# Kernel optimization log

Hardware: AMD Instinct MI355X
Metric: run time of the kernel (lower is better)

The kernel has to match this reference:

```python
import jax, jax.numpy as jnp
import numpy as np

THRESH = 1.0
TAU_M = 20.0
TAU_S = 5.0
NUM_STEPS = 300
LENS = 0.5  # boxcar surrogate half-width for the spike Heaviside

@jax.custom_vjp
def act_fun(x):
    # Heaviside spike with boxcar surrogate gradient (as in BPTC-NOSO ActFun)
    return (x > 0.0).astype(x.dtype)

def _act_fwd(x):
    return act_fun(x), x

def _act_bwd(x, g):
    return (g * (jnp.abs(x) < LENS).astype(g.dtype),)

act_fun.defvjp(_act_fwd, _act_bwd)

@jax.custom_vjp
def dodt(spike, dt):
    # forward: spike * (step - num_steps); backward: surrogate do/dt = -spike
    return spike * dt

def _dodt_fwd(spike, dt):
    return spike * dt, spike

def _dodt_bwd(spike, g):
    return (-g * spike, jnp.zeros((), g.dtype))

dodt.defvjp(_dodt_fwd, _dodt_bwd)

def setup_inputs() -> dict:
    key = jax.random.key(0)
    k1, k2, k3 = jax.random.split(key, 3)
    B = 256
    N_IN, N_H, N_OUT = 2 * 34 * 34, 800, 10
    # binary event spikes like N-MNIST (sparse-ish)
    inp = (jax.random.uniform(k1, (B, 2, 34, 34, NUM_STEPS)) < 0.1).astype(jnp.float32)
    w1 = jax.random.normal(k2, (N_H, N_IN), jnp.float32) * np.float32(np.sqrt(2.0 / N_IN))
    w2 = jax.random.normal(k3, (N_OUT, N_H), jnp.float32) * np.float32(np.sqrt(2.0 / N_H))
    return {"input": inp, "w1": w1, "w2": w2, "batch_size": B}

def _forward(input, w1, w2, batch_size):
    B = batch_size
    N_IN, N_H, N_OUT = w1.shape[1], w1.shape[0], w2.shape[0]
    dm = jnp.float32(np.exp(-1.0 / TAU_M))
    ds = jnp.float32(np.exp(-1.0 / TAU_S))
    x_t = jnp.moveaxis(input.reshape(B, N_IN, NUM_STEPS), -1, 0)  # [T, B, N_IN]

    z = lambda n: jnp.zeros((B, n), jnp.float32)
    o = lambda n: jnp.ones((B, n), jnp.float32)
    carry = (z(N_IN), z(N_IN), o(N_H),          # vm1, vs1, sav1
             z(N_H), z(N_H), o(N_OUT),          # vm2, vs2, sav2
             NUM_STEPS * jnp.ones((B, N_OUT), jnp.float32),  # out_t
             z(N_OUT),                           # out_u
             jnp.zeros((3,), jnp.float32))       # sum_sp

    def step(c, xs):
        vm1, vs1, sav1, vm2, vs2, sav2, out_t, out_u, sum_sp = c
        step_f, in_spike = xs
        # layer 1: dual-exponential synapse traces on input, NOSO (one spike) gating
        vm1 = dm * vm1 + in_spike
        vs1 = ds * vs1 + in_spike
        u1 = sav1 * ((vm1 - vs1) @ w1.T)        # um - us fused into one GEMM
        spk1 = act_fun(u1 - THRESH)
        sav1 = sav1 * (1.0 - spk1)
        # layer 2 (output neurons)
        vm2 = dm * vm2 + spk1
        vs2 = ds * vs2 + spk1
        u2 = sav2 * ((vm2 - vs2) @ w2.T)
        spk2 = act_fun(u2 - THRESH)
        sav2 = sav2 * (1.0 - spk2)
        out_t = out_t + dodt(spk2, step_f - NUM_STEPS)  # records first-spike time
        out_u = out_u + spk2 * u2
        sum_sp = sum_sp + jax.lax.stop_gradient(
            jnp.stack([in_spike.sum(), spk1.sum(), spk2.sum()]))
        return (vm1, vs1, sav1, vm2, vs2, sav2, out_t, out_u, sum_sp), None

    steps = jnp.arange(NUM_STEPS, dtype=jnp.float32)
    c, _ = jax.lax.scan(step, carry, (steps, x_t))
    return c[6], c[7], c[8]

def reference(input, w1, w2, batch_size):
    return _forward(input, w1, w2, batch_size)
```

## Files before the change

### kernel.cpp

```cpp
#include <hip/hip_runtime.h>
#include <hip/hip_bf16.h>

typedef unsigned int u32;
typedef unsigned short u16;

#define BATCH 256
#define TSTEPS 300
#define N_IN 2312
#define N_H 800
#define N_OUT 10
#define KW 74
#define KREAL 2368
#define KSTEPS 74
#define MTOT (BATCH * TSTEPS)
#define ROWB 9472

#define BM 128
#define BN 160

typedef __attribute__((ext_vector_type(8))) short bf16x8;
typedef __attribute__((ext_vector_type(4))) float f32x4;

static inline size_t alignup(size_t x) { return (x + 255) & ~(size_t)255; }

__device__ __forceinline__ void gl_lds16(const void* g, void* l) {
    __builtin_amdgcn_global_load_lds(
        (const __attribute__((address_space(1))) unsigned int*)g,
        (__attribute__((address_space(3))) unsigned int*)l,
        16, 0, 0);
}

__global__ void init_k(u32* cnts) {
    if (threadIdx.x < 4) cnts[threadIdx.x] = 0;
}

__global__ __launch_bounds__(256) void prep_w(const float* __restrict__ w1,
                                              u32* __restrict__ Wc) {
    int idx = blockIdx.x * 256 + threadIdx.x;
    if (idx >= N_H * KREAL) return;
    int h = idx / KREAL, k = idx - h * KREAL;
    float w = (k < N_IN) ? w1[(size_t)h * N_IN + k] : 0.0f;
    __hip_bfloat16 hb = __float2bfloat16(w);
    float hf = __bfloat162float(hb);
    __hip_bfloat16 lb = __float2bfloat16(w - hf);
    u32 val = (u32)(*(u16*)&hb) | ((u32)(*(u16*)&lb) << 16);
    Wc[(size_t)h * KREAL + k] = val;
}

__global__ __launch_bounds__(256) void prep_x(const float* __restrict__ X,
                                              u32* __restrict__ XB,
                                              u32* __restrict__ cnts,
                                              int b0) {
    int bl = blockIdx.x;
    int b = b0 + bl;
    int tc = blockIdx.y;
    int t0 = tc * 64;
    int nrows = min(64, TSTEPS - t0);
    __shared__ u32 bits[64][76];
    int tid = threadIdx.x;
    int tl = tid & 63;
    int wg = tid >> 6;
    int t = t0 + tl;
    bool tvalid = (tl < nrows);
    u32 pc = 0;
    for (int j = 0; j < 19; ++j) {
        int w = wg + 4 * j;
        if (w >= KW) break;
        u32 reg = 0;
        if (w < 73 && tvalid) {
            int ibase = w * 32;
            int nb = min(32, N_IN - ibase);
            const float* xp = X + ((size_t)b * N_IN + ibase) * TSTEPS + t;
            for (int bit = 0; bit < nb; ++bit) {
                float v = xp[(size_t)bit * TSTEPS];
                reg |= (v > 0.5f) ? (1u << bit) : 0u;
            }
        }
        pc += __popc(reg);
        bits[tl][w] = reg;
    }
    for (int off = 32; off; off >>= 1) pc += __shfl_down(pc, off);
    if ((tid & 63) == 0 && pc) atomicAdd(cnts + 0, pc);
    __syncthreads();
    int total = nrows * KW;
    u32* outp = XB + (size_t)(bl * TSTEPS + t0) * KW;
    for (int idx = tid; idx < total; idx += 256) {
        int r = idx / KW, w = idx - r * KW;
        outp[idx] = bits[r][w];
    }
}

__global__ __launch_bounds__(256, 4) void gemm_k(const u32* __restrict__ XB,
                                                 const u16* __restrict__ Wc,
                                                 float* __restrict__ C1,
                                                 int nwg, int mblocks) {
    int d = blockIdx.y * 5 + blockIdx.x;
    int xcd = d & 7, jj = d >> 3;
    int q = nwg >> 3, r = nwg & 7;
    int lid = (xcd < r ? xcd * (q + 1) : r * (q + 1) + (xcd - r) * q) + jj;
    int nb = lid / mblocks, mb = lid - nb * mblocks;
    int m0 = mb * BM, n0 = nb * BN;

    __shared__ __align__(16) u16 Bs[2][BN * 64];

    int tid = threadIdx.x, lane = tid & 63, w = tid >> 6;
    int wm = w >> 1, wn = w & 1;

    const char* srcB[5];
#pragma unroll
    for (int i = 0; i < 5; ++i) {
        int slot = w * 5120 + i * 1024 + lane * 16;
        int row = slot >> 7, c = (slot >> 4) & 7;
        srcB[i] = (const char*)Wc + (size_t)(n0 + row) * ROWB + (size_t)((c ^ (row & 7)) << 4);
    }
    char* ldsB = (char*)&Bs[0][0] + w * 5120;

    int r0 = wm * 64 + (lane & 15);
    const u32* pAm0 = XB + (size_t)(m0 + r0) * KW;
    const u32* pAm1 = pAm0 + 16 * KW;
    const u32* pAm2 = pAm0 + 32 * KW;
    const u32* pAm3 = pAm0 + 48 * KW;
    int sh0 = (lane >> 4) * 4;

    f32x4 acc[4][5] = {};

#pragma unroll
    for (int i = 0; i < 5; ++i) { gl_lds16(srcB[i], ldsB + i * 1024); srcB[i] += 128; }
    __syncthreads();

    for (int ks = 0; ks < KSTEPS; ++ks) {
        int buf = ks & 1;
        if (ks < KSTEPS - 1) {
            char* dst = ldsB + (buf ^ 1) * 20480;
#pragma unroll
            for (int i = 0; i < 5; ++i) { gl_lds16(srcB[i], dst + i * 1024); srcB[i] += 128; }
        }
        u32 wv0 = pAm0[ks], wv1 = pAm1[ks], wv2 = pAm2[ks], wv3 = pAm3[ks];
        const u16* bsb = &Bs[buf][0];
#pragma unroll
        for (int kk = 0; kk < 2; ++kk) {
            u32 wv[4] = {wv0, wv1, wv2, wv3};
            bf16x8 af[4];
#pragma unroll
            for (int mi = 0; mi < 4; ++mi) {
                u32 nib = wv[mi] >> (kk * 16 + sh0);
                uint4 ax;
                ax.x = (nib & 1u) ? 0x3F803F80u : 0u;
                ax.y = (nib & 2u) ? 0x3F803F80u : 0u;
                ax.z = (nib & 4u) ? 0x3F803F80u : 0u;
                ax.w = (nib & 8u) ? 0x3F803F80u : 0u;
                af[mi] = *reinterpret_cast<bf16x8*>(&ax);
            }
            __builtin_amdgcn_s_setprio(1);
#pragma unroll
            for (int ni = 0; ni < 5; ++ni) {
                int rr = wn * 80 + ni * 16 + (lane & 15);
                bf16x8 bf = *reinterpret_cast<const bf16x8*>(
                    &bsb[(rr << 6) + ((((kk << 2) + (lane >> 4)) ^ (rr & 7)) << 3)]);
#pragma unroll
                for (int mi = 0; mi < 4; ++mi)
                    acc[mi][ni] = __builtin_amdgcn_mfma_f32_16x16x32_bf16(af[mi], bf, acc[mi][ni], 0, 0, 0);
            }
            __builtin_amdgcn_s_setprio(0);
        }
        __syncthreads();
    }

#pragma unroll
    for (int mi = 0; mi < 4; ++mi)
#pragma unroll
        for (int ni = 0; ni < 5; ++ni) {
            int col = n0 + wn * 80 + ni * 16 + (lane & 15);
            int rowb = m0 + wm * 64 + mi * 16 + ((lane >> 4) << 2);
#pragma unroll
            for (int j = 0; j < 4; ++j)
                C1[(size_t)(rowb + j) * N_H + col] = acc[mi][ni][j];
        }
}

__global__ __launch_bounds__(256) void spike1_k(const float* __restrict__ C1,
                                                u16* __restrict__ T1,
                                                u32* __restrict__ cnts,
                                                int b0) {
    const float dm = 0.95122942450071400910f;
    const float ds = 0.81873075307798185867f;
    int bl = blockIdx.x, b = b0 + bl, tid = threadIdx.x;
    const float* cbase = C1 + (size_t)bl * TSTEPS * N_H;
    bool h3ok = (tid < N_H - 768);
    float M[4] = {0, 0, 0, 0}, S[4] = {0, 0, 0, 0};
    int t1v[4] = {TSTEPS, TSTEPS, TSTEPS, TSTEPS};

    auto ld = [&](float* dst, int tt) {
        if (tt < TSTEPS) {
            const float* p = cbase + (size_t)tt * N_H;
            dst[0] = p[tid]; dst[1] = p[tid + 256]; dst[2] = p[tid + 512];
            dst[3] = h3ok ? p[tid + 768] : 0.0f;
        } else { dst[0] = dst[1] = dst[2] = dst[3] = 0.0f; }
    };
    auto step = [&](const float* cc, int t) {
#pragma unroll
        for (int r = 0; r < 4; ++r) {
            M[r] = dm * M[r] + cc[r];
            S[r] = ds * S[r] + cc[r];
            float u = M[r] - S[r];
            if (u > 1.0f && t < t1v[r]) t1v[r] = t;
        }
    };

    float c0[4], c1_[4], c2_[4], c3_[4];
    ld(c0, 0); ld(c1_, 1); ld(c2_, 2); ld(c3_, 3);
    for (int t = 0; t < TSTEPS; t += 4) {
        float n0[4], n1[4], n2[4], n3[4];
        ld(n0, t + 4); ld(n1, t + 5); ld(n2, t + 6); ld(n3, t + 7);
        step(c0, t); step(c1_, t + 1); step(c2_, t + 2); step(c3_, t + 3);
#pragma unroll
        for (int r = 0; r < 4; ++r) { c0[r] = n0[r]; c1_[r] = n1[r]; c2_[r] = n2[r]; c3_[r] = n3[r]; }
    }

    u16* tp = T1 + (size_t)b * N_H;
    tp[tid] = (u16)t1v[0];
    tp[tid + 256] = (u16)t1v[1];
    tp[tid + 512] = (u16)t1v[2];
    if (h3ok) tp[tid + 768] = (u16)t1v[3];

    u32 cnt = (u32)(t1v[0] < TSTEPS) + (u32)(t1v[1] < TSTEPS) + (u32)(t1v[2] < TSTEPS)
            + (u32)(h3ok && t1v[3] < TSTEPS);
    for (int off = 32; off; off >>= 1) cnt += __shfl_down(cnt, off);
    if ((tid & 63) == 0 && cnt) atomicAdd(cnts + 1, cnt);
}

__global__ __launch_bounds__(320) void out_k(const u16* __restrict__ T1,
                                             const float* __restrict__ w2,
                                             float* __restrict__ out,
                                             u32* __restrict__ cnts) {
    const float dm = 0.95122942450071400910f;
    const float ds = 0.81873075307798185867f;
    int b = blockIdx.x, tid = threadIdx.x;
    __shared__ float w2s[N_OUT * N_H];
    __shared__ u16 t1s[N_H];
    __shared__ float Rs[TSTEPS][N_OUT];
    for (int i = tid; i < N_OUT * N_H; i += 320) w2s[i] = w2[i];
    for (int i = tid; i < N_H; i += 320) t1s[i] = T1[(size_t)b * N_H + i];
    __syncthreads();
    if (tid < TSTEPS) {
        float R[N_OUT];
#pragma unroll
        for (int o = 0; o < N_OUT; ++o) R[o] = 0.0f;
        for (int h = 0; h < N_H; ++h) {
            if ((int)t1s[h] == tid) {
#pragma unroll
                for (int o = 0; o < N_OUT; ++o) R[o] += w2s[o * N_H + h];
            }
        }
#pragma unroll
        for (int o = 0; o < N_OUT; ++o) Rs[tid][o] = R[o];
    }
    __syncthreads();
    if (tid < N_OUT) {
        float vm = 0.0f, vs = 0.0f, sav = 1.0f, ot = (float)TSTEPS, ou = 0.0f;
        u32 c2 = 0;
        for (int t = 0; t < TSTEPS; ++t) {
            float rr = Rs[t][tid];
            vm = dm * vm + rr;
            vs = ds * vs + rr;
            float u2 = sav * (vm - vs);
            float spk = (u2 - 1.0f > 0.0f) ? 1.0f : 0.0f;
            sav *= (1.0f - spk);
            ot += spk * ((float)t - (float)TSTEPS);
            ou += spk * u2;
            c2 += (u32)spk;
        }
        out[b * N_OUT + tid] = ot;
        out[BATCH * N_OUT + b * N_OUT + tid] = ou;
        if (c2) atomicAdd(cnts + 2, c2);
    }
}

__global__ void fin_k(const u32* cnts, float* out) {
    if (threadIdx.x == 0) {
        out[2 * BATCH * N_OUT + 0] = (float)cnts[0];
        out[2 * BATCH * N_OUT + 1] = (float)cnts[1];
        out[2 * BATCH * N_OUT + 2] = (float)cnts[2];
    }
}

extern "C" void kernel_launch(void* const* d_in, const int* in_sizes, int n_in,
                              void* d_out, int out_size, void* d_ws, size_t ws_size,
                              hipStream_t stream) {
    (void)in_sizes; (void)n_in; (void)out_size;
    const float* X  = (const float*)d_in[0];
    const float* w1 = (const float*)d_in[1];
    const float* w2 = (const float*)d_in[2];
    float* out = (float*)d_out;
    char* ws = (char*)d_ws;

    const size_t WC_BYTES = (size_t)N_H * KREAL * 4;
    const size_t T1_BYTES = (size_t)BATCH * N_H * 2;

    int nch = 1;
    for (; nch <= 8; nch *= 2) {
        size_t xbb = (size_t)(MTOT / nch) * KW * 4;
        size_t c1b = (size_t)(MTOT / nch) * N_H * 4;
        size_t tot = alignup(xbb) + alignup(c1b) + alignup(WC_BYTES) + alignup(T1_BYTES) + 256;
        if (tot <= ws_size) break;
    }
    if (nch > 8) nch = 8;
    int bchunk = BATCH / nch;
    int mcount = bchunk * TSTEPS;
    int mblocks = mcount / BM;
    int nwg = 5 * mblocks;

    size_t off = 0;
    u32* XB   = (u32*)(ws + off);   off += alignup((size_t)mcount * KW * 4);
    float* C1 = (float*)(ws + off); off += alignup((size_t)mcount * N_H * 4);
    u32* Wc   = (u32*)(ws + off);   off += alignup(WC_BYTES);
    u16* T1   = (u16*)(ws + off);   off += alignup(T1_BYTES);
    u32* cnts = (u32*)(ws + off);

    init_k<<<1, 64, 0, stream>>>(cnts);
    prep_w<<<(N_H * KREAL) / 256, 256, 0, stream>>>(w1, Wc);

    for (int c = 0; c < nch; ++c) {
        int b0 = c * bchunk;
        prep_x<<<dim3(bchunk, 5), 256, 0, stream>>>(X, XB, cnts, b0);
        gemm_k<<<dim3(5, mblocks), 256, 0, stream>>>(XB, (const u16*)Wc, C1, nwg, mblocks);
        spike1_k<<<bchunk, 256, 0, stream>>>(C1, T1, cnts, b0);
    }
    out_k<<<BATCH, 320, 0, stream>>>(T1, w2, out, cnts);
    fin_k<<<1, 64, 0, stream>>>(cnts, out);
}
```

Measured before the change: 857.4 us.

## Transpose bit-packed input, deepen GEMM prefetch, and split spike scan across blocks

The packed input bits are now stored K-major (transposed), so the GEMM reads A words with coalesced, stride-contiguous loads one k-step ahead. B tiles are prefetched two stages ahead with explicit vmcnt waits and raw barriers in place of __syncthreads. The spike scan kernel now spreads hidden neurons over four blocks per batch row, one neuron per thread, to raise parallelism. The risks are that the manual waitcnt depends on an exact count of outstanding loads, and that 56 of 256 threads per spike block sit idle.

Measured after the change: 935.6 us. 9.1% more time.

```diff
diff --git a/kernel.cpp b/kernel.cpp
--- a/kernel.cpp
+++ b/kernel.cpp
@@ -17,6 +17,7 @@
 
 #define BM 128
 #define BN 160
+#define BUFB (BN * 64 * 2)
 
 typedef __attribute__((ext_vector_type(8))) short bf16x8;
 typedef __attribute__((ext_vector_type(4))) float f32x4;
@@ -48,9 +49,9 @@
 }
 
 __global__ __launch_bounds__(256) void prep_x(const float* __restrict__ X,
-                                              u32* __restrict__ XB,
+                                              u32* __restrict__ XBT,
                                               u32* __restrict__ cnts,
-                                              int b0) {
+                                              int b0, int mcount) {
     int bl = blockIdx.x;
     int b = b0 + bl;
     int tc = blockIdx.y;
@@ -82,18 +83,17 @@
     for (int off = 32; off; off >>= 1) pc += __shfl_down(pc, off);
     if ((tid & 63) == 0 && pc) atomicAdd(cnts + 0, pc);
     __syncthreads();
-    int total = nrows * KW;
-    u32* outp = XB + (size_t)(bl * TSTEPS + t0) * KW;
-    for (int idx = tid; idx < total; idx += 256) {
-        int r = idx / KW, w = idx - r * KW;
-        outp[idx] = bits[r][w];
-    }
-}
-
-__global__ __launch_bounds__(256, 4) void gemm_k(const u32* __restrict__ XB,
+    if (tvalid) {
+        int m = bl * TSTEPS + t0 + tl;
+        for (int w = wg; w < KW; w += 4)
+            XBT[(size_t)w * mcount + m] = bits[tl][w];
+    }
+}
+
+__global__ __launch_bounds__(256, 4) void gemm_k(const u32* __restrict__ XBT,
                                                  const u16* __restrict__ Wc,
                                                  float* __restrict__ C1,
-                                                 int nwg, int mblocks) {
+                                                 int nwg, int mblocks, int mcount) {
     int d = blockIdx.y * 5 + blockIdx.x;
     int xcd = d & 7, jj = d >> 3;
     int q = nwg >> 3, r = nwg & 7;
@@ -113,33 +113,27 @@
         int row = slot >> 7, c = (slot >> 4) & 7;
         srcB[i] = (const char*)Wc + (size_t)(n0 + row) * ROWB + (size_t)((c ^ (row & 7)) << 4);
     }
-    char* ldsB = (char*)&Bs[0][0] + w * 5120;
-
-    int r0 = wm * 64 + (lane & 15);
-    const u32* pAm0 = XB + (size_t)(m0 + r0) * KW;
-    const u32* pAm1 = pAm0 + 16 * KW;
-    const u32* pAm2 = pAm0 + 32 * KW;
-    const u32* pAm3 = pAm0 + 48 * KW;
+    char* ldsQ = (char*)&Bs[0][0] + w * 5120;
+
+    const u32* pA = XBT + m0 + wm * 64 + (lane & 15);
     int sh0 = (lane >> 4) * 4;
 
     f32x4 acc[4][5] = {};
 
 #pragma unroll
-    for (int i = 0; i < 5; ++i) { gl_lds16(srcB[i], ldsB + i * 1024); srcB[i] += 128; }
-    __syncthreads();
+    for (int i = 0; i < 5; ++i) { gl_lds16(srcB[i], ldsQ + i * 1024); srcB[i] += 128; }
+    u32 a0 = pA[0], a1 = pA[16], a2 = pA[32], a3 = pA[48];
+    pA += mcount;
+#pragma unroll
+    for (int i = 0; i < 5; ++i) { gl_lds16(srcB[i], ldsQ + BUFB + i * 1024); srcB[i] += 128; }
 
     for (int ks = 0; ks < KSTEPS; ++ks) {
-        int buf = ks & 1;
-        if (ks < KSTEPS - 1) {
-            char* dst = ldsB + (buf ^ 1) * 20480;
-#pragma unroll
-            for (int i = 0; i < 5; ++i) { gl_lds16(srcB[i], dst + i * 1024); srcB[i] += 128; }
-        }
-        u32 wv0 = pAm0[ks], wv1 = pAm1[ks], wv2 = pAm2[ks], wv3 = pAm3[ks];
-        const u16* bsb = &Bs[buf][0];
+        asm volatile("s_waitcnt vmcnt(9)" ::: "memory");
+        __builtin_amdgcn_s_barrier();
+        u32 wv[4] = {a0, a1, a2, a3};
+        const u16* bsb = &Bs[ks & 1][0];
 #pragma unroll
         for (int kk = 0; kk < 2; ++kk) {
-            u32 wv[4] = {wv0, wv1, wv2, wv3};
             bf16x8 af[4];
 #pragma unroll
             for (int mi = 0; mi < 4; ++mi) {
@@ -163,7 +157,17 @@
             }
             __builtin_amdgcn_s_setprio(0);
         }
-        __syncthreads();
+        asm volatile("" ::: "memory");
+        __builtin_amdgcn_s_barrier();
+        if (ks + 1 < KSTEPS) {
+            a0 = pA[0]; a1 = pA[16]; a2 = pA[32]; a3 = pA[48];
+            pA += mcount;
+        }
+        if (ks + 2 < KSTEPS) {
+            char* dst = (char*)&Bs[0][0] + (ks & 1) * BUFB + w * 5120;
+#pragma unroll
+            for (int i = 0; i < 5; ++i) { gl_lds16(srcB[i], dst + i * 1024); srcB[i] += 128; }
+        }
     }
 
 #pragma unroll
@@ -185,46 +189,34 @@
     const float dm = 0.95122942450071400910f;
     const float ds = 0.81873075307798185867f;
     int bl = blockIdx.x, b = b0 + bl, tid = threadIdx.x;
-    const float* cbase = C1 + (size_t)bl * TSTEPS * N_H;
-    bool h3ok = (tid < N_H - 768);
-    float M[4] = {0, 0, 0, 0}, S[4] = {0, 0, 0, 0};
-    int t1v[4] = {TSTEPS, TSTEPS, TSTEPS, TSTEPS};
-
-    auto ld = [&](float* dst, int tt) {
-        if (tt < TSTEPS) {
-            const float* p = cbase + (size_t)tt * N_H;
-            dst[0] = p[tid]; dst[1] = p[tid + 256]; dst[2] = p[tid + 512];
-            dst[3] = h3ok ? p[tid + 768] : 0.0f;
-        } else { dst[0] = dst[1] = dst[2] = dst[3] = 0.0f; }
-    };
-    auto step = [&](const float* cc, int t) {
+    int h = blockIdx.y * 200 + tid;
+    bool act = (tid < 200);
+    const float* cp = C1 + (size_t)bl * TSTEPS * N_H + (act ? h : 0);
+    float M = 0.0f, S = 0.0f;
+    int t1 = TSTEPS;
+
+    float c[4];
+#pragma unroll
+    for (int r = 0; r < 4; ++r) c[r] = cp[(size_t)r * N_H];
+    for (int t = 0; t < TSTEPS; t += 4) {
+        float n[4];
 #pragma unroll
         for (int r = 0; r < 4; ++r) {
-            M[r] = dm * M[r] + cc[r];
-            S[r] = ds * S[r] + cc[r];
-            float u = M[r] - S[r];
-            if (u > 1.0f && t < t1v[r]) t1v[r] = t;
-        }
-    };
-
-    float c0[4], c1_[4], c2_[4], c3_[4];
-    ld(c0, 0); ld(c1_, 1); ld(c2_, 2); ld(c3_, 3);
-    for (int t = 0; t < TSTEPS; t += 4) {
-        float n0[4], n1[4], n2[4], n3[4];
-        ld(n0, t + 4); ld(n1, t + 5); ld(n2, t + 6); ld(n3, t + 7);
-        step(c0, t); step(c1_, t + 1); step(c2_, t + 2); step(c3_, t + 3);
-#pragma unroll
-        for (int r = 0; r < 4; ++r) { c0[r] = n0[r]; c1_[r] = n1[r]; c2_[r] = n2[r]; c3_[r] = n3[r]; }
-    }
-
-    u16* tp = T1 + (size_t)b * N_H;
-    tp[tid] = (u16)t1v[0];
-    tp[tid + 256] = (u16)t1v[1];
-    tp[tid + 512] = (u16)t1v[2];
-    if (h3ok) tp[tid + 768] = (u16)t1v[3];
-
-    u32 cnt = (u32)(t1v[0] < TSTEPS) + (u32)(t1v[1] < TSTEPS) + (u32)(t1v[2] < TSTEPS)
-            + (u32)(h3ok && t1v[3] < TSTEPS);
+            int tt = t + 4 + r;
+            n[r] = (tt < TSTEPS) ? cp[(size_t)tt * N_H] : 0.0f;
+        }
+#pragma unroll
+        for (int r = 0; r < 4; ++r) {
+            M = dm * M + c[r];
+            S = ds * S + c[r];
+            if (M - S > 1.0f && t + r < t1) t1 = t + r;
+        }
+#pragma unroll
+        for (int r = 0; r < 4; ++r) c[r] = n[r];
+    }
+
+    if (act) T1[(size_t)b * N_H + h] = (u16)t1;
+    u32 cnt = (act && t1 < TSTEPS) ? 1u : 0u;
     for (int off = 32; off; off >>= 1) cnt += __shfl_down(cnt, off);
     if ((tid & 63) == 0 && cnt) atomicAdd(cnts + 1, cnt);
 }
@@ -311,7 +303,7 @@
     int nwg = 5 * mblocks;
 
     size_t off = 0;
-    u32* XB   = (u32*)(ws + off);   off += alignup((size_t)mcount * KW * 4);
+    u32* XBT  = (u32*)(ws + off);   off += alignup((size_t)mcount * KW * 4);
     float* C1 = (float*)(ws + off); off += alignup((size_t)mcount * N_H * 4);
     u32* Wc   = (u32*)(ws + off);   off += alignup(WC_BYTES);
     u16* T1   = (u16*)(ws + off);   off += alignup(T1_BYTES);
@@ -322,9 +314,9 @@
 
     for (int c = 0; c < nch; ++c) {
         int b0 = c * bchunk;
-        prep_x<<<dim3(bchunk, 5), 256, 0, stream>>>(X, XB, cnts, b0);
-        gemm_k<<<dim3(5, mblocks), 256, 0, stream>>>(XB, (const u16*)Wc, C1, nwg, mblocks);
-        spike1_k<<<bchunk, 256, 0, stream>>>(C1, T1, cnts, b0);
+        prep_x<<<dim3(bchunk, 5), 256, 0, stream>>>(X, XBT, cnts, b0, mcount);
+        gemm_k<<<dim3(5, mblocks), 256, 0, stream>>>(XBT, (const u16*)Wc, C1, nwg, mblocks, mcount);
+        spike1_k<<<dim3(bchunk, 4), 256, 0, stream>>>(C1, T1, cnts, b0);
     }
     out_k<<<BATCH, 320, 0, stream>>>(T1, w2, out, cnts);
     fin_k<<<1, 64, 0, stream>>>(cnts, out);
```
